# Performance work log

Hardware: AMD Instinct MI355X
Metric: run time of the kernel (lower is better)

The kernel has to match this reference:

```python
import jax, jax.numpy as jnp
import numpy as np

B, T, I, H = 64, 512, 1024, 1024  # batch, seq_len, input_size, hidden_size


def setup_inputs() -> dict:
    key = jax.random.key(0)
    ks = jax.random.split(key, 5)
    s = 0.02
    return {
        "sequence": jax.random.normal(ks[0], (B, T, I), jnp.float32),
        "Wx0": jax.random.normal(ks[1], (4 * H, I), jnp.float32) * s,
        "Wh0": jax.random.normal(ks[2], (4 * H, H), jnp.float32) * s,
        "b0": jnp.zeros((4 * H,), jnp.float32),
        "Wx1": jax.random.normal(ks[3], (4 * H, H), jnp.float32) * s,
        "Wh1": jax.random.normal(ks[4], (4 * H, H), jnp.float32) * s,
        "b1": jnp.zeros((4 * H,), jnp.float32),
    }


def _run_layer(xs, Wx, Wh, b):
    # xs: [T, B, D_in]; packed gates order: forget, input-gate(w), candidate(i), output(m)
    batch = xs.shape[1]
    hid = Wh.shape[1]
    # precompute input projections for all timesteps: [T, B, 4H]
    xproj = jnp.einsum('tbd,gd->tbg', xs, Wx) + b

    def step(carry, xp):
        c, h = carry
        z = xp + h @ Wh.T  # [B, 4H]
        f, w, i, m = jnp.split(z, 4, axis=-1)
        c = c * jax.nn.sigmoid(f) + jax.nn.sigmoid(w) * jnp.tanh(i)
        h = jnp.tanh(c) * jax.nn.sigmoid(m)
        return (c, h), h

    init = (jnp.zeros((batch, hid), xs.dtype), jnp.zeros((batch, hid), xs.dtype))
    (c, h), hs = jax.lax.scan(step, init, xproj)
    return hs, h  # hs: [T, B, H], h: [B, H]


def reference(sequence, Wx0, Wh0, b0, Wx1, Wh1, b1):
    xs = jnp.transpose(sequence, (1, 0, 2))  # [T, B, I]
    hs0, _ = _run_layer(xs, Wx0, Wh0, b0)
    _, h_last = _run_layer(hs0, Wx1, Wh1, b1)
    return h_last  # [B, H] == H[:, :, -1] of the original
```

## Files before the change

### kernel.cpp

```cpp
#include <hip/hip_runtime.h>

typedef __bf16 bf16x8 __attribute__((ext_vector_type(8)));
typedef float f32x4 __attribute__((ext_vector_type(4)));
typedef unsigned long long u64;

__device__ inline float sigm(float x) { return 1.0f / (1.0f + __expf(-x)); }
__device__ inline float tanh_f(float x) {
    float e = __expf(2.0f * x);
    return 1.0f - 2.0f / (e + 1.0f);
}

__device__ inline unsigned short f2bf(float f) {
    __bf16 h = (__bf16)f;
    return __builtin_bit_cast(unsigned short, h);
}

__device__ inline bf16x8 cvt8(float4 lo, float4 hi) {
    bf16x8 r;
    r[0] = (__bf16)lo.x; r[1] = (__bf16)lo.y; r[2] = (__bf16)lo.z; r[3] = (__bf16)lo.w;
    r[4] = (__bf16)hi.x; r[5] = (__bf16)hi.y; r[6] = (__bf16)hi.z; r[7] = (__bf16)hi.w;
    return r;
}

__device__ inline u64 ld64c(const u64* p) {
    return __hip_atomic_load(p, __ATOMIC_RELAXED, __HIP_MEMORY_SCOPE_AGENT);
}
__device__ inline void st32c(unsigned int* p, unsigned int v) {
    __hip_atomic_store(p, v, __ATOMIC_RELAXED, __HIP_MEMORY_SCOPE_AGENT);
}
__device__ inline unsigned int ld32c(const unsigned int* p) {
    return __hip_atomic_load(p, __ATOMIC_RELAXED, __HIP_MEMORY_SCOPE_AGENT);
}


__global__ void cvt_weights(const float* __restrict__ Wx0, const float* __restrict__ Wh0,
                            const float* __restrict__ Wx1, const float* __restrict__ Wh1,
                            unsigned short* __restrict__ W0, unsigned short* __restrict__ W1) {
    size_t idx = ((size_t)blockIdx.x * 256 + threadIdx.x) * 8;
    const size_t LSZ = (size_t)4096 * 2048;
    int layer = idx >= LSZ;
    size_t e = idx - (layer ? LSZ : 0);
    int row = (int)(e >> 11);
    int k = (int)(e & 2047);
    const float* src = layer ? (k < 1024 ? Wx1 : Wh1) : (k < 1024 ? Wx0 : Wh0);
    const float* s = src + (size_t)row * 1024 + (k & 1023);
    float4 lo = ((const float4*)s)[0], hi = ((const float4*)s)[1];
    *reinterpret_cast<bf16x8*>((layer ? W1 : W0) + e) = cvt8(lo, hi);
}

__global__ void cvt_seq(const float* __restrict__ seq, unsigned short* __restrict__ seqb, int T) {
    int t = blockIdx.x >> 6, b = blockIdx.x & 63;
    int row = b & 31, btile = b >> 5, tid = threadIdx.x;
    const float* s = seq + ((size_t)b * T + t) * 1024 + tid * 8;
    float4 lo = ((const float4*)s)[0], hi = ((const float4*)s)[1];
    int off = ((row >> 4) << 14) + ((tid >> 2) << 9) + (((tid & 3) << 4) + (row & 15)) * 8;
    *reinterpret_cast<bf16x8*>(seqb + ((size_t)t * 2 + btile) * 32768 + off) = cvt8(lo, hi);
}

union SmemU {
    unsigned short a[2][32768];
    float z[4][32][16];
};

struct StageRegs { u64 q[32]; };

__device__ inline void stage_issue(StageRegs& r, const unsigned short* __restrict__ src) {
#pragma unroll
    for (int i = 0; i < 16; ++i) {
        const u64* s = (const u64*)(src + (size_t)((threadIdx.x + (i << 8)) << 3));
        r.q[2 * i] = ld64c(s);
        r.q[2 * i + 1] = ld64c(s + 1);
    }
}

__device__ inline void stage_issue_plain(StageRegs& r, const unsigned short* __restrict__ src) {
#pragma unroll
    for (int i = 0; i < 16; ++i) {
        const u64* s = (const u64*)(src + (size_t)((threadIdx.x + (i << 8)) << 3));
        r.q[2 * i] = s[0];
        r.q[2 * i + 1] = s[1];
    }
}

__device__ inline void stage_write(const StageRegs& r, unsigned short* tile) {
#pragma unroll
    for (int i = 0; i < 16; ++i) {
        u64* d = (u64*)(tile + (size_t)((threadIdx.x + (i << 8)) << 3));
        d[0] = r.q[2 * i];
        d[1] = r.q[2 * i + 1];
    }
}

template <int BASE>
__device__ inline void mfma_pass(const unsigned short* tile, const bf16x8 (&w)[64],
                                 f32x4& acc0, f32x4& acc1, int lane) {
#pragma unroll
    for (int kk = 0; kk < 32; ++kk) {
        bf16x8 av0 = *(const bf16x8*)(tile + kk * 512 + lane * 8);
        bf16x8 av1 = *(const bf16x8*)(tile + 16384 + kk * 512 + lane * 8);
        acc0 = __builtin_amdgcn_mfma_f32_16x16x32_bf16(av0, w[BASE + kk], acc0, 0, 0, 0);
        acc1 = __builtin_amdgcn_mfma_f32_16x16x32_bf16(av1, w[BASE + kk], acc1, 0, 0, 0);
    }
}

template <bool SEQB>
__global__ __launch_bounds__(256, 1) void lstm_persistent(
    const float* __restrict__ seq, const unsigned short* __restrict__ seqb,
    const unsigned short* __restrict__ W0, const unsigned short* __restrict__ W1,
    const float* __restrict__ bias0, const float* __restrict__ bias1,
    unsigned short* h0buf, unsigned short* h1buf, unsigned int* flags,
    float* out, int T) {
    const int bid = blockIdx.x;
    const int r = bid & 7, q = bid >> 3;
    const int btile = q & 1, t2 = q >> 1;
    const int layer = t2 >> 3;
    const int jtile = ((t2 & 7) << 3) | r;
    const int j0 = jtile * 16;
    const int brow = btile * 32;

    const int tid = threadIdx.x;
    const int wave = tid >> 6, lane = tid & 63;
    const int ln15 = lane & 15, lhi = lane >> 4;

    const unsigned short* Wl = layer ? W1 : W0;
    const float* bias = layer ? bias1 : bias0;
    const unsigned short* Bbase = Wl + (size_t)(wave * 1024 + j0 + ln15) * 2048 + lhi * 8;
    unsigned short* hown = layer ? h1buf : h0buf;

    __shared__ SmemU smem;

    bf16x8 wreg[64];
#pragma unroll
    for (int q2 = 0; q2 < 64; ++q2)
        wreg[q2] = *reinterpret_cast<const bf16x8*>(Bbase + q2 * 32);

    const int bl = tid >> 3;
    const int jj = (tid & 7) * 2;
    const float bf0 = bias[j0 + jj],        bf1 = bias[j0 + jj + 1];
    const float bw0 = bias[1024 + j0 + jj], bw1 = bias[1024 + j0 + jj + 1];
    const float bi0 = bias[2048 + j0 + jj], bi1 = bias[2048 + j0 + jj + 1];
    const float bm0 = bias[3072 + j0 + jj], bm1 = bias[3072 + j0 + jj + 1];
    const int colg = j0 + jj;
    const int hoff = ((bl >> 4) << 14) + ((colg >> 5) << 9) +
                     ((((colg >> 3) & 3) << 4) + (bl & 15)) * 8 + (colg & 7);

    float creg0 = 0.f, creg1 = 0.f;
    const int P = T + 2;

    for (int p = 0; p < P; ++p) {
        const bool act = layer ? (p >= 2) : (p < T);
        const int t = layer ? (p - 2) : p;
        const bool have0 = act && (layer == 1 || SEQB);

        if (have0) {
            StageRegs s0;
            if (layer == 0)
                stage_issue_plain(s0, seqb + ((size_t)t * 2 + btile) * 32768);
            else
                stage_issue(s0, h0buf + (size_t)((t % 3) * 2 + btile) * 32768);
            stage_write(s0, smem.a[0]);
        }

        if (p > 0) {
            const unsigned int tgt = (unsigned int)p;
            unsigned int pv = ld32c(&flags[tid]);
            while (pv < tgt) { __builtin_amdgcn_s_sleep(1); pv = ld32c(&flags[tid]); }
        }
        __syncthreads();

        if (act) {
            f32x4 acc0 = {0.f, 0.f, 0.f, 0.f};
            f32x4 acc1 = {0.f, 0.f, 0.f, 0.f};

            StageRegs s1;
            const unsigned short* hsrc = layer
                ? h1buf + (size_t)(((t + 1) & 1) * 2 + btile) * 32768
                : h0buf + (size_t)(((t + 2) % 3) * 2 + btile) * 32768;
            stage_issue(s1, hsrc);

            if (layer == 0 && !SEQB) {
                const float* a0f = seq + ((size_t)(brow + ln15) * T + t) * 1024 + lhi * 8;
                const float* a1f = a0f + (size_t)16 * T * 1024;
#pragma unroll
                for (int kk = 0; kk < 32; ++kk) {
                    float4 l0 = ((const float4*)a0f)[0], h0v = ((const float4*)a0f)[1];
                    float4 l1 = ((const float4*)a1f)[0], h1v = ((const float4*)a1f)[1];
                    bf16x8 av0 = cvt8(l0, h0v), av1 = cvt8(l1, h1v);
                    acc0 = __builtin_amdgcn_mfma_f32_16x16x32_bf16(av0, wreg[kk], acc0, 0, 0, 0);
                    acc1 = __builtin_amdgcn_mfma_f32_16x16x32_bf16(av1, wreg[kk], acc1, 0, 0, 0);
                    a0f += 32; a1f += 32;
                }
            } else {
                mfma_pass<0>(smem.a[0], wreg, acc0, acc1, lane);
            }

            stage_write(s1, smem.a[1]);
            __syncthreads();
            mfma_pass<32>(smem.a[1], wreg, acc0, acc1, lane);

#pragma unroll
            for (int rr = 0; rr < 4; ++rr) {
                smem.z[wave][4 * lhi + rr][ln15] = acc0[rr];
                smem.z[wave][16 + 4 * lhi + rr][ln15] = acc1[rr];
            }
            __syncthreads();

            {
                float2 zf = *(const float2*)&smem.z[0][bl][jj];
                float2 zw = *(const float2*)&smem.z[1][bl][jj];
                float2 zi = *(const float2*)&smem.z[2][bl][jj];
                float2 zm = *(const float2*)&smem.z[3][bl][jj];
                float c0n = creg0 * sigm(zf.x + bf0) + sigm(zw.x + bw0) * tanh_f(zi.x + bi0);
                float c1n = creg1 * sigm(zf.y + bf1) + sigm(zw.y + bw1) * tanh_f(zi.y + bi1);
                float h0v = tanh_f(c0n) * sigm(zm.x + bm0);
                float h1v = tanh_f(c1n) * sigm(zm.y + bm1);
                creg0 = c0n; creg1 = c1n;
                const int wbuf = layer ? (t & 1) : (t % 3);
                unsigned short* tb = hown + (size_t)(wbuf * 2 + btile) * 32768;
                unsigned int packed = (unsigned int)f2bf(h0v) | ((unsigned int)f2bf(h1v) << 16);
                st32c((unsigned int*)(tb + hoff), packed);
                if (layer && t == T - 1) {
                    int idx = (brow + bl) * 1024 + colg;
                    out[idx] = h0v; out[idx + 1] = h1v;
                }
            }
        }

        if (p < P - 1) {
            __syncthreads();
            if (tid == 0) st32c(&flags[bid], (unsigned int)(p + 1));
        }
    }
}

extern "C" void kernel_launch(void* const* d_in, const int* in_sizes, int n_in,
                              void* d_out, int out_size, void* d_ws, size_t ws_size,
                              hipStream_t stream) {
    const float* seq = (const float*)d_in[0];
    const float* Wx0 = (const float*)d_in[1];
    const float* Wh0 = (const float*)d_in[2];
    const float* b0 = (const float*)d_in[3];
    const float* Wx1 = (const float*)d_in[4];
    const float* Wh1 = (const float*)d_in[5];
    const float* b1 = (const float*)d_in[6];
    float* out = (float*)d_out;
    char* ws = (char*)d_ws;
    const int T = 512;

    const size_t WBYTES = (size_t)4096 * 2048 * 2;
    const size_t SEQB_BYTES = (size_t)512 * 2 * 32768 * 2;
    const size_t H0_BYTES = 3 * 2 * 65536;
    const size_t H1_BYTES = 2 * 2 * 65536;
    const size_t STATE_BYTES = H0_BYTES + H1_BYTES + 1024;

    size_t offSeqb = 2 * WBYTES;
    bool big = ws_size >= 2 * WBYTES + SEQB_BYTES + STATE_BYTES;
    size_t offState = big ? (offSeqb + SEQB_BYTES) : offSeqb;

    unsigned short* W0p = (unsigned short*)(ws);
    unsigned short* W1p = (unsigned short*)(ws + WBYTES);
    unsigned short* seqbp = (unsigned short*)(ws + offSeqb);
    unsigned short* h0p = (unsigned short*)(ws + offState);
    unsigned short* h1p = (unsigned short*)(ws + offState + H0_BYTES);
    unsigned int* flagsp = (unsigned int*)(ws + offState + H0_BYTES + H1_BYTES);

    hipLaunchKernelGGL(cvt_weights, dim3(8192), dim3(256), 0, stream,
                       Wx0, Wh0, Wx1, Wh1, W0p, W1p);
    if (big)
        hipLaunchKernelGGL(cvt_seq, dim3(T * 64), dim3(128), 0, stream, seq, seqbp, T);
    hipMemsetAsync(ws + offState, 0, STATE_BYTES, stream);

    int Tv = T;
    void* args[] = {&seq, &seqbp, &W0p, &W1p, &b0, &b1, &h0p, &h1p, &flagsp, &out, &Tv};
    if (big) {
        hipError_t e = hipLaunchCooperativeKernel((void*)lstm_persistent<true>,
                                                  dim3(256), dim3(256), args, 0, stream);
        if (e != hipSuccess) {
            hipLaunchKernelGGL((lstm_persistent<true>), dim3(256), dim3(256), 0, stream,
                               seq, seqbp, W0p, W1p, b0, b1, h0p, h1p, flagsp, out, Tv);
        }
    } else {
        hipError_t e = hipLaunchCooperativeKernel((void*)lstm_persistent<false>,
                                                  dim3(256), dim3(256), args, 0, stream);
        if (e != hipSuccess) {
            hipLaunchKernelGGL((lstm_persistent<false>), dim3(256), dim3(256), 0, stream,
                               seq, seqbp, W0p, W1p, b0, b1, h0p, h1p, flagsp, out, Tv);
        }
    }
}
```

Baseline: 3.927 ms.

## Use per-wave flags, deeper h0 ring, and let layer 0 run ahead

Each wave now publishes its own completion flag after waiting on its outstanding stores, replacing the block-wide barrier before the flag write. Each waiting thread polls the four wave flags of one block with two 64-bit loads. The layer-0 h0 ring buffer grows from 3 to 5 slots so layer-0 blocks can run up to two steps ahead of layer 1, which loosens the cross-layer lockstep. The smem union becomes a struct so the staging area and gate scratch no longer alias. This costs more LDS, more workspace and a more intricate ordering protocol.

```diff
diff --git a/kernel.cpp b/kernel.cpp
--- a/kernel.cpp
+++ b/kernel.cpp
@@ -27,9 +27,6 @@
 }
 __device__ inline void st32c(unsigned int* p, unsigned int v) {
     __hip_atomic_store(p, v, __ATOMIC_RELAXED, __HIP_MEMORY_SCOPE_AGENT);
-}
-__device__ inline unsigned int ld32c(const unsigned int* p) {
-    return __hip_atomic_load(p, __ATOMIC_RELAXED, __HIP_MEMORY_SCOPE_AGENT);
 }
 
 
@@ -57,7 +54,7 @@
     *reinterpret_cast<bf16x8*>(seqb + ((size_t)t * 2 + btile) * 32768 + off) = cvt8(lo, hi);
 }
 
-union SmemU {
+struct Smem {
     unsigned short a[2][32768];
     float z[4][32][16];
 };
@@ -127,7 +124,7 @@
     const unsigned short* Bbase = Wl + (size_t)(wave * 1024 + j0 + ln15) * 2048 + lhi * 8;
     unsigned short* hown = layer ? h1buf : h0buf;
 
-    __shared__ SmemU smem;
+    __shared__ Smem smem;
 
     bf16x8 wreg[64];
 #pragma unroll
@@ -144,6 +141,9 @@
     const int hoff = ((bl >> 4) << 14) + ((colg >> 5) << 9) +
                      ((((colg >> 3) & 3) << 4) + (bl & 15)) * 8 + (colg & 7);
 
+    const int tgt_bias = (layer == 0 && tid >= 128) ? 2 : 0;
+    const u64* myflagq = (const u64*)&flags[tid * 4];
+
     float creg0 = 0.f, creg1 = 0.f;
     const int P = T + 2;
 
@@ -157,14 +157,22 @@
             if (layer == 0)
                 stage_issue_plain(s0, seqb + ((size_t)t * 2 + btile) * 32768);
             else
-                stage_issue(s0, h0buf + (size_t)((t % 3) * 2 + btile) * 32768);
+                stage_issue(s0, h0buf + (size_t)((t % 5) * 2 + btile) * 32768);
             stage_write(s0, smem.a[0]);
         }
 
-        if (p > 0) {
-            const unsigned int tgt = (unsigned int)p;
-            unsigned int pv = ld32c(&flags[tid]);
-            while (pv < tgt) { __builtin_amdgcn_s_sleep(1); pv = ld32c(&flags[tid]); }
+        {
+            const int tgt = p - tgt_bias;
+            if (tgt > 0) {
+                for (;;) {
+                    u64 a = ld64c(myflagq), b = ld64c(myflagq + 1);
+                    unsigned int m0 = (unsigned int)a, m1 = (unsigned int)(a >> 32);
+                    unsigned int m2 = (unsigned int)b, m3 = (unsigned int)(b >> 32);
+                    unsigned int mn = min(min(m0, m1), min(m2, m3));
+                    if ((int)mn >= tgt) break;
+                    __builtin_amdgcn_s_sleep(1);
+                }
+            }
         }
         __syncthreads();
 
@@ -175,7 +183,7 @@
             StageRegs s1;
             const unsigned short* hsrc = layer
                 ? h1buf + (size_t)(((t + 1) & 1) * 2 + btile) * 32768
-                : h0buf + (size_t)(((t + 2) % 3) * 2 + btile) * 32768;
+                : h0buf + (size_t)(((t + 4) % 5) * 2 + btile) * 32768;
             stage_issue(s1, hsrc);
 
             if (layer == 0 && !SEQB) {
@@ -215,7 +223,7 @@
                 float h0v = tanh_f(c0n) * sigm(zm.x + bm0);
                 float h1v = tanh_f(c1n) * sigm(zm.y + bm1);
                 creg0 = c0n; creg1 = c1n;
-                const int wbuf = layer ? (t & 1) : (t % 3);
+                const int wbuf = layer ? (t & 1) : (t % 5);
                 unsigned short* tb = hown + (size_t)(wbuf * 2 + btile) * 32768;
                 unsigned int packed = (unsigned int)f2bf(h0v) | ((unsigned int)f2bf(h1v) << 16);
                 st32c((unsigned int*)(tb + hoff), packed);
@@ -227,8 +235,8 @@
         }
 
         if (p < P - 1) {
-            __syncthreads();
-            if (tid == 0) st32c(&flags[bid], (unsigned int)(p + 1));
+            asm volatile("s_waitcnt vmcnt(0)" ::: "memory");
+            if (lane == 0) st32c(&flags[bid * 4 + wave], (unsigned int)(p + 1));
         }
     }
 }
@@ -249,9 +257,10 @@
 
     const size_t WBYTES = (size_t)4096 * 2048 * 2;
     const size_t SEQB_BYTES = (size_t)512 * 2 * 32768 * 2;
-    const size_t H0_BYTES = 3 * 2 * 65536;
+    const size_t H0_BYTES = 5 * 2 * 65536;
     const size_t H1_BYTES = 2 * 2 * 65536;
-    const size_t STATE_BYTES = H0_BYTES + H1_BYTES + 1024;
+    const size_t FLAG_BYTES = 4096;
+    const size_t STATE_BYTES = H0_BYTES + H1_BYTES + FLAG_BYTES;
 
     size_t offSeqb = 2 * WBYTES;
     bool big = ws_size >= 2 * WBYTES + SEQB_BYTES + STATE_BYTES;
```

New measurement: 4.577 ms. 16.6% more time.
